# Kernel optimization log

Hardware: AMD Instinct MI355X
Metric: run time of the kernel (lower is better)

## Reference

```python
import jax, jax.numpy as jnp
import numpy as np

OBS_LEN = 8
PRED_LEN = 12
BATCH = 65536
EMB = 64
H = 64


def setup_inputs() -> dict:
    key = jax.random.key(0)
    ks = jax.random.split(key, 18)
    s = 1.0 / np.sqrt(H)  # torch default uniform bound scale, used as std here

    def p(k, shape):
        return (jax.random.normal(k, shape, dtype=jnp.float32) * s).astype(jnp.float32)

    return {
        "obs_traj": jax.random.normal(ks[0], (OBS_LEN, BATCH, 2), dtype=jnp.float32),
        "obs_traj_rel": jax.random.normal(ks[1], (OBS_LEN, BATCH, 2), dtype=jnp.float32),
        # encoder params
        "enc_emb_w": p(ks[2], (EMB, 2)),
        "enc_emb_b": p(ks[3], (EMB,)),
        "enc_w_ih": p(ks[4], (4 * H, EMB)),
        "enc_w_hh": p(ks[5], (4 * H, H)),
        "enc_b_ih": p(ks[6], (4 * H,)),
        "enc_b_hh": p(ks[7], (4 * H,)),
        # decoder params
        "dec_emb_w": p(ks[8], (EMB, 2)),
        "dec_emb_b": p(ks[9], (EMB,)),
        "dec_w_ih": p(ks[10], (4 * H, EMB)),
        "dec_w_hh": p(ks[11], (4 * H, H)),
        "dec_b_ih": p(ks[12], (4 * H,)),
        "dec_b_hh": p(ks[13], (4 * H,)),
        "h2p_w": p(ks[14], (2, H)),
        "h2p_b": p(ks[15], (2,)),
    }


def _lstm_cell(h, c, x, w_ih, w_hh, b_ih, b_hh):
    # torch nn.LSTM gate order: i, f, g, o
    gates = x @ w_ih.T + h @ w_hh.T + (b_ih + b_hh)
    i, f, g, o = jnp.split(gates, 4, axis=-1)
    c_new = jax.nn.sigmoid(f) * c + jax.nn.sigmoid(i) * jnp.tanh(g)
    h_new = jax.nn.sigmoid(o) * jnp.tanh(c_new)
    return h_new, c_new


def reference(obs_traj, obs_traj_rel,
              enc_emb_w, enc_emb_b, enc_w_ih, enc_w_hh, enc_b_ih, enc_b_hh,
              dec_emb_w, dec_emb_b, dec_w_ih, dec_w_hh, dec_b_ih, dec_b_hh,
              h2p_w, h2p_b):
    batch = obs_traj_rel.shape[1]

    # ---------- Encoder ----------
    enc_in = obs_traj_rel @ enc_emb_w.T + enc_emb_b  # [T, B, EMB]

    def enc_step(carry, x_t):
        h, c = carry
        h, c = _lstm_cell(h, c, x_t, enc_w_ih, enc_w_hh, enc_b_ih, enc_b_hh)
        return (h, c), None

    h0 = jnp.zeros((batch, H), dtype=obs_traj_rel.dtype)
    c0 = jnp.zeros((batch, H), dtype=obs_traj_rel.dtype)
    (h_enc, _), _ = jax.lax.scan(enc_step, (h0, c0), enc_in)

    # ---------- Decoder ----------
    dec_h = h_enc                                   # final encoder hidden seeds decoder
    dec_c = jnp.zeros((batch, H), dtype=obs_traj_rel.dtype)
    last_pos_rel = obs_traj_rel[-1]
    dec_in = last_pos_rel @ dec_emb_w.T + dec_emb_b  # [B, EMB]

    def dec_step(carry, _):
        h, c, x = carry
        h, c = _lstm_cell(h, c, x, dec_w_ih, dec_w_hh, dec_b_ih, dec_b_hh)
        rel_pos = h @ h2p_w.T + h2p_b               # [B, 2]
        x_next = rel_pos @ dec_emb_w.T + dec_emb_b  # [B, EMB]
        return (h, c, x_next), rel_pos

    (_, _, _), pred_traj_fake_rel = jax.lax.scan(
        dec_step, (dec_h, dec_c, dec_in), None, length=PRED_LEN)
    return pred_traj_fake_rel  # [PRED_LEN, B, 2]
```

## Files before the change

kernel.cpp:

```cpp
#include <hip/hip_runtime.h>

#define OBS_LEN 8
#define PRED_LEN 12
#define TILE_B 64
#define NTHREADS 256

typedef __attribute__((ext_vector_type(8))) short short8;
typedef __attribute__((ext_vector_type(4))) float floatx4;
typedef __attribute__((ext_vector_type(2))) float floatx2;
typedef __attribute__((ext_vector_type(2))) unsigned int u32x2;
typedef unsigned short u16;
typedef unsigned int u32;

#define L2E 1.442695040888963f

__device__ __forceinline__ u16 f2bf(float f) {
  __bf16 b = (__bf16)f;
  return __builtin_bit_cast(u16, b);
}

#if __has_builtin(__builtin_amdgcn_exp2f)
__device__ __forceinline__ float fexp2_(float x) { return __builtin_amdgcn_exp2f(x); }
#else
__device__ __forceinline__ float fexp2_(float x) { return exp2f(x); }
#endif
__device__ __forceinline__ floatx2 exp2v(floatx2 x) {
  floatx2 r;
  r.x = fexp2_(x.x);
  r.y = fexp2_(x.y);
  return r;
}
#if __has_builtin(__builtin_amdgcn_rcpf)
__device__ __forceinline__ floatx2 rcp2(floatx2 x) {
  floatx2 r;
  r.x = __builtin_amdgcn_rcpf(x.x);
  r.y = __builtin_amdgcn_rcpf(x.y);
  return r;
}
#else
__device__ __forceinline__ floatx2 rcp2(floatx2 x) {
  return floatx2{1.0f / x.x, 1.0f / x.y};
}
#endif

__device__ __forceinline__ floatx4 mfma_bf(short8 a, short8 b, floatx4 c) {
  return __builtin_amdgcn_mfma_f32_16x16x32_bf16(a, b, c, 0, 0, 0);
}

__device__ __forceinline__ void load_afrags(const float* __restrict__ W,
                                            short8 (&af)[4][2],
                                            int u0, int q, int l16) {
#pragma unroll
  for (int t = 0; t < 4; ++t)
#pragma unroll
    for (int kf = 0; kf < 2; ++kf) {
      const float* src = W + (t * 64 + u0 + l16) * 64 + kf * 32 + q * 8;
      const floatx4 w0 = *(const floatx4*)src;
      const floatx4 w1 = *(const floatx4*)(src + 4);
      short8 a;
#pragma unroll
      for (int j = 0; j < 4; ++j) {
        a[j] = (short)f2bf(w0[j]);
        a[j + 4] = (short)f2bf(w1[j]);
      }
      af[t][kf] = a;
    }
}

__device__ __forceinline__ void load_afrags_eff(const float* __restrict__ Whh,
                                                const float* __restrict__ aS0,
                                                const float* __restrict__ aS1,
                                                const float* __restrict__ hw0,
                                                const float* __restrict__ hw1,
                                                short8 (&af)[4][2],
                                                int u0, int q, int l16) {
#pragma unroll
  for (int t = 0; t < 4; ++t) {
    const int g = t * 64 + u0 + l16;
    const float a0 = aS0[g], a1 = aS1[g];
#pragma unroll
    for (int kf = 0; kf < 2; ++kf) {
      const int u = kf * 32 + q * 8;
      const float* src = Whh + g * 64 + u;
      const floatx4 w0 = *(const floatx4*)src;
      const floatx4 w1 = *(const floatx4*)(src + 4);
      const floatx4 p00 = *(const floatx4*)(hw0 + u);
      const floatx4 p01 = *(const floatx4*)(hw0 + u + 4);
      const floatx4 p10 = *(const floatx4*)(hw1 + u);
      const floatx4 p11 = *(const floatx4*)(hw1 + u + 4);
      short8 a;
#pragma unroll
      for (int j = 0; j < 4; ++j) {
        a[j] = (short)f2bf(w0[j] + a0 * p00[j] + a1 * p10[j]);
        a[j + 4] = (short)f2bf(w1[j] + a0 * p01[j] + a1 * p11[j]);
      }
      af[t][kf] = a;
    }
  }
}

__device__ __forceinline__ void fold_rank2(const float* __restrict__ wr,
                                           const float* __restrict__ emb_w,
                                           const float* __restrict__ emb_b,
                                           float& A0, float& A1, float& B0) {
  A0 = A1 = B0 = 0.f;
#pragma unroll
  for (int e4 = 0; e4 < 16; ++e4) {
    const floatx4 w = *(const floatx4*)(wr + e4 * 4);
    const floatx4 m0 = *(const floatx4*)(emb_w + e4 * 8);
    const floatx4 m1 = *(const floatx4*)(emb_w + e4 * 8 + 4);
    const floatx4 bb = *(const floatx4*)(emb_b + e4 * 4);
    A0 += w[0] * m0[0] + w[1] * m0[2] + w[2] * m1[0] + w[3] * m1[2];
    A1 += w[0] * m0[1] + w[1] * m0[3] + w[2] * m1[1] + w[3] * m1[3];
    B0 += w[0] * bb[0] + w[1] * bb[1] + w[2] * bb[2] + w[3] * bb[3];
  }
}

__device__ __forceinline__ void build_gfrag(const float* __restrict__ A0t,
                                            const float* __restrict__ A1t,
                                            short8 (&xf)[4],
                                            int u0, int q, int l16) {
#pragma unroll
  for (int t = 0; t < 4; ++t) {
    short8 a = short8{0, 0, 0, 0, 0, 0, 0, 0};
    if (q == 0) {
      const int g = t * 64 + u0 + l16;
      a[0] = (short)f2bf(A0t[g]);
      a[1] = (short)f2bf(A1t[g]);
    }
    xf[t] = a;
  }
}

__device__ __forceinline__ void nonlin_store(const floatx4 (&acc)[4],
                                             floatx2 (&c2)[2],
                                             u16* __restrict__ wrh,
                                             int s, int q, int wv) {
  const int sw = s & 7;
  u32 hpk[2];
#pragma unroll
  for (int p = 0; p < 2; ++p) {
    const floatx2 iv = {acc[0][2 * p], acc[0][2 * p + 1]};
    const floatx2 fv = {acc[1][2 * p], acc[1][2 * p + 1]};
    const floatx2 gv = {acc[2][2 * p], acc[2][2 * p + 1]};
    const floatx2 ov = {acc[3][2 * p], acc[3][2 * p + 1]};
    const floatx2 ei = exp2v(iv * -L2E);
    const floatx2 ef = exp2v(fv * -L2E);
    const floatx2 eg = exp2v(gv * (2.0f * L2E));
    const floatx2 eo = exp2v(ov * -L2E);
    const floatx2 A = ei + 1.0f;
    const floatx2 F = ef + 1.0f;
    const floatx2 Bg = eg + 1.0f;
    const floatx2 P = A * Bg;
    const floatx2 num = c2[p] * P + (eg - 1.0f) * F;
    const floatx2 cn = num * rcp2(F * P);
    c2[p] = cn;
    const floatx2 ec = exp2v(cn * (2.0f * L2E));
    const floatx2 h = (ec - 1.0f) * rcp2((eo + 1.0f) * (ec + 1.0f));
    hpk[p] = (u32)f2bf(h.x) | ((u32)f2bf(h.y) << 16);
  }
  *(u32x2*)(wrh + s * 64 + (((wv * 2 + (q >> 1)) ^ sw) * 8) + (q & 1) * 4) =
      u32x2{hpk[0], hpk[1]};
}

__device__ __forceinline__ void cell_step_fold(
    const u16* __restrict__ rdh, u16* __restrict__ wrh,
    const short8 (&afh)[4][2], const short8 (&xf)[4],
    const float* __restrict__ biasrow, const float* __restrict__ posrow,
    floatx2 (&c)[4][2], int q, int l16, int wv, int u0) {
#pragma unroll
  for (int n = 0; n < 4; ++n) {
    const int s = n * 16 + l16, sw = s & 7;
    const u16* hr = rdh + s * 64;
    const short8 hb0 = *(const short8*)(hr + ((q ^ sw) * 8));
    const short8 hb1 = *(const short8*)(hr + (((q + 4) ^ sw) * 8));
    const floatx2 pp = *(const floatx2*)(posrow + s * 2);
    short8 pf = short8{0, 0, 0, 0, 0, 0, 0, 0};
    if (q == 0) {
      pf[0] = (short)f2bf(pp.x);
      pf[1] = (short)f2bf(pp.y);
    }
    floatx4 acc[4];
#pragma unroll
    for (int t = 0; t < 4; ++t) {
      const floatx4 bias = *(const floatx4*)(biasrow + t * 64 + u0 + q * 4);
      acc[t] = mfma_bf(xf[t], pf, bias);
    }
#pragma unroll
    for (int t = 0; t < 4; ++t) acc[t] = mfma_bf(afh[t][0], hb0, acc[t]);
#pragma unroll
    for (int t = 0; t < 4; ++t) acc[t] = mfma_bf(afh[t][1], hb1, acc[t]);
    nonlin_store(acc, c[n], wrh, s, q, wv);
  }
}

__device__ __forceinline__ void dec_step_folded(
    const u16* __restrict__ rdh, u16* __restrict__ wrh,
    const short8 (&af)[4][2], const short8 (&xf)[4],
    const float* __restrict__ biasrow, float b2p0, float b2p1,
    float* __restrict__ relrow,
    floatx2 (&c)[4][2], int q, int l16, int wv, int u0) {
#pragma unroll
  for (int n = 0; n < 4; ++n) {
    const int s = n * 16 + l16, sw = s & 7;
    const u16* hr = rdh + s * 64;
    const short8 hb0 = *(const short8*)(hr + ((q ^ sw) * 8));
    const short8 hb1 = *(const short8*)(hr + (((q + 4) ^ sw) * 8));
    floatx4 acc[4];
#pragma unroll
    for (int t = 0; t < 4; ++t) {
      const floatx4 bias = *(const floatx4*)(biasrow + t * 64 + u0 + q * 4);
      acc[t] = mfma_bf(af[t][0], hb0, bias);
    }
#pragma unroll
    for (int t = 0; t < 4; ++t) acc[t] = mfma_bf(af[t][1], hb1, acc[t]);
    if (wv == n) {
      floatx4 ar = mfma_bf(xf[0], hb0, floatx4{0.f, 0.f, 0.f, 0.f});
      ar = mfma_bf(xf[1], hb1, ar);
      if (q == 0)
        *(floatx2*)(relrow + s * 2) = floatx2{ar[0] + b2p0, ar[1] + b2p1};
    }
    nonlin_store(acc, c[n], wrh, s, q, wv);
  }
}

__global__ void __launch_bounds__(NTHREADS, 4)
lstm_kernel(const float* __restrict__ obs_rel,
            const float* __restrict__ enc_emb_w, const float* __restrict__ enc_emb_b,
            const float* __restrict__ enc_w_ih, const float* __restrict__ enc_w_hh,
            const float* __restrict__ enc_b_ih, const float* __restrict__ enc_b_hh,
            const float* __restrict__ dec_emb_w, const float* __restrict__ dec_emb_b,
            const float* __restrict__ dec_w_ih, const float* __restrict__ dec_w_hh,
            const float* __restrict__ dec_b_ih, const float* __restrict__ dec_b_hh,
            const float* __restrict__ h2p_w, const float* __restrict__ h2p_b,
            float* __restrict__ out, int batch) {
  __shared__ __align__(16) u16 hS[2][TILE_B * 64];
  __shared__ __align__(16) float posS[OBS_LEN][TILE_B * 2];
  __shared__ __align__(16) float biasS[3][256];
  __shared__ __align__(16) float eA0[256], eA1[256];
  __shared__ __align__(16) float dA0[256], dA1[256];
  __shared__ __align__(16) float hw0S[64], hw1S[64];
  __shared__ __align__(16) float relS[PRED_LEN][TILE_B * 2];

  const int tid = threadIdx.x;
  const int wv = tid >> 6, lane = tid & 63;
  const int q = lane >> 4, l16 = lane & 15;
  const int u0 = wv << 4;
  const long S0 = (long)blockIdx.x * TILE_B;

  {
    const int t = tid >> 5, i = tid & 31;
    *(floatx4*)&posS[t][i * 4] =
        *(const floatx4*)(obs_rel + (long)t * batch * 2 + S0 * 2 + i * 4);
  }
  if (tid < 64) {
    hw0S[tid] = h2p_w[tid];
    hw1S[tid] = h2p_w[64 + tid];
  }
  {
    float A0, A1, B0;
    fold_rank2(enc_w_ih + tid * 64, enc_emb_w, enc_emb_b, A0, A1, B0);
    eA0[tid] = A0;
    eA1[tid] = A1;
    biasS[0][tid] = enc_b_ih[tid] + enc_b_hh[tid] + B0;
    fold_rank2(dec_w_ih + tid * 64, dec_emb_w, dec_emb_b, A0, A1, B0);
    dA0[tid] = A0;
    dA1[tid] = A1;
    const float db = dec_b_ih[tid] + dec_b_hh[tid] + B0;
    biasS[1][tid] = db;
    biasS[2][tid] = db + A0 * h2p_b[0] + A1 * h2p_b[1];
  }
  for (int i = tid; i < TILE_B * 64 / 2; i += NTHREADS) ((u32*)&hS[0][0])[i] = 0;

  short8 afh[4][2], xf[4];
  floatx2 c[4][2];
  load_afrags(enc_w_hh, afh, u0, q, l16);
#pragma unroll
  for (int n = 0; n < 4; ++n) c[n][0] = c[n][1] = floatx2{0.f, 0.f};
  const float b2p0 = h2p_b[0], b2p1 = h2p_b[1];
  __syncthreads();
  build_gfrag(eA0, eA1, xf, u0, q, l16);

  int pb = 0;
#pragma unroll 1
  for (int t = 0; t < OBS_LEN; ++t) {
    cell_step_fold(hS[pb], hS[pb ^ 1], afh, xf, &biasS[0][0], &posS[t][0], c,
                   q, l16, wv, u0);
    __syncthreads();
    pb ^= 1;
  }

  load_afrags(dec_w_hh, afh, u0, q, l16);
  build_gfrag(dA0, dA1, xf, u0, q, l16);
#pragma unroll
  for (int n = 0; n < 4; ++n) c[n][0] = c[n][1] = floatx2{0.f, 0.f};
  cell_step_fold(hS[pb], hS[pb ^ 1], afh, xf, &biasS[1][0], &posS[7][0], c,
                 q, l16, wv, u0);
  load_afrags_eff(dec_w_hh, dA0, dA1, hw0S, hw1S, afh, u0, q, l16);
#pragma unroll
  for (int kf = 0; kf < 2; ++kf) {
    const int kb = kf * 32 + q * 8;
    short8 a;
#pragma unroll
    for (int j = 0; j < 4; ++j) {
      const float r0 = (l16 == 0) ? hw0S[kb + j] : (l16 == 1) ? hw1S[kb + j] : 0.f;
      const float r1 =
          (l16 == 0) ? hw0S[kb + 4 + j] : (l16 == 1) ? hw1S[kb + 4 + j] : 0.f;
      a[j] = (short)f2bf(r0);
      a[j + 4] = (short)f2bf(r1);
    }
    xf[kf] = a;
  }
  __syncthreads();
  pb ^= 1;

#pragma unroll 1
  for (int j = 1; j < PRED_LEN; ++j) {
    dec_step_folded(hS[pb], hS[pb ^ 1], afh, xf, &biasS[2][0], b2p0, b2p1,
                    &relS[j - 1][0], c, q, l16, wv, u0);
    __syncthreads();
    pb ^= 1;
  }

  {
    const int s = wv * 16 + l16, sw = s & 7;
    const u16* hr = hS[pb] + s * 64;
    const short8 ha = *(const short8*)(hr + ((q ^ sw) * 8));
    const short8 hc = *(const short8*)(hr + (((q + 4) ^ sw) * 8));
    floatx4 ar = mfma_bf(xf[0], ha, floatx4{0.f, 0.f, 0.f, 0.f});
    ar = mfma_bf(xf[1], hc, ar);
    if (q == 0)
      *(floatx2*)(&relS[PRED_LEN - 1][s * 2]) =
          floatx2{ar[0] + b2p0, ar[1] + b2p1};
  }
  __syncthreads();

#pragma unroll
  for (int r = 0; r < 6; ++r) {
    const int f = tid + r * 256;
    const int j = f >> 7, e = f & 127;
    out[(long)j * batch * 2 + S0 * 2 + e] = ((const float*)relS)[f];
  }
}

extern "C" void kernel_launch(void* const* d_in, const int* in_sizes, int n_in,
                              void* d_out, int out_size, void* d_ws, size_t ws_size,
                              hipStream_t stream) {
  const float* obs_rel = (const float*)d_in[1];
  const int batch = in_sizes[1] / (OBS_LEN * 2);

  const int blocks = batch / TILE_B;
  hipLaunchKernelGGL(lstm_kernel, dim3(blocks), dim3(NTHREADS), 0, stream,
                     obs_rel,
                     (const float*)d_in[2], (const float*)d_in[3],
                     (const float*)d_in[4], (const float*)d_in[5],
                     (const float*)d_in[6], (const float*)d_in[7],
                     (const float*)d_in[8], (const float*)d_in[9],
                     (const float*)d_in[10], (const float*)d_in[11],
                     (const float*)d_in[12], (const float*)d_in[13],
                     (const float*)d_in[14], (const float*)d_in[15],
                     (float*)d_out, batch);
}
```

Baseline: 200.0 us.

## Give each wave its own batch rows and stage weight fragments in LDS

Each wave now owns 16 batch rows and computes all 256 gate units for them, so the hidden state lives in a per-wave LDS region. This removes the per-timestep __syncthreads barriers. Weight fragments are pre-swizzled into shared memory and read per MFMA rather than held in registers, and the launch bound drops from 4 to 3 blocks per SM. Predictions are written straight to global memory instead of being staged in LDS. The trade-off is more LDS traffic per step and lower occupancy, in exchange for fewer barriers and less register pressure.

Measured after the change: 197.7 us. Within noise of the previous version (-1.2%).

```diff
diff --git a/kernel.cpp b/kernel.cpp
--- a/kernel.cpp
+++ b/kernel.cpp
@@ -8,6 +8,7 @@
 typedef __attribute__((ext_vector_type(8))) short short8;
 typedef __attribute__((ext_vector_type(4))) float floatx4;
 typedef __attribute__((ext_vector_type(2))) float floatx2;
+typedef __attribute__((ext_vector_type(4))) unsigned int u32x4;
 typedef __attribute__((ext_vector_type(2))) unsigned int u32x2;
 typedef unsigned short u16;
 typedef unsigned int u32;
@@ -47,56 +48,8 @@
   return __builtin_amdgcn_mfma_f32_16x16x32_bf16(a, b, c, 0, 0, 0);
 }
 
-__device__ __forceinline__ void load_afrags(const float* __restrict__ W,
-                                            short8 (&af)[4][2],
-                                            int u0, int q, int l16) {
-#pragma unroll
-  for (int t = 0; t < 4; ++t)
-#pragma unroll
-    for (int kf = 0; kf < 2; ++kf) {
-      const float* src = W + (t * 64 + u0 + l16) * 64 + kf * 32 + q * 8;
-      const floatx4 w0 = *(const floatx4*)src;
-      const floatx4 w1 = *(const floatx4*)(src + 4);
-      short8 a;
-#pragma unroll
-      for (int j = 0; j < 4; ++j) {
-        a[j] = (short)f2bf(w0[j]);
-        a[j + 4] = (short)f2bf(w1[j]);
-      }
-      af[t][kf] = a;
-    }
-}
-
-__device__ __forceinline__ void load_afrags_eff(const float* __restrict__ Whh,
-                                                const float* __restrict__ aS0,
-                                                const float* __restrict__ aS1,
-                                                const float* __restrict__ hw0,
-                                                const float* __restrict__ hw1,
-                                                short8 (&af)[4][2],
-                                                int u0, int q, int l16) {
-#pragma unroll
-  for (int t = 0; t < 4; ++t) {
-    const int g = t * 64 + u0 + l16;
-    const float a0 = aS0[g], a1 = aS1[g];
-#pragma unroll
-    for (int kf = 0; kf < 2; ++kf) {
-      const int u = kf * 32 + q * 8;
-      const float* src = Whh + g * 64 + u;
-      const floatx4 w0 = *(const floatx4*)src;
-      const floatx4 w1 = *(const floatx4*)(src + 4);
-      const floatx4 p00 = *(const floatx4*)(hw0 + u);
-      const floatx4 p01 = *(const floatx4*)(hw0 + u + 4);
-      const floatx4 p10 = *(const floatx4*)(hw1 + u);
-      const floatx4 p11 = *(const floatx4*)(hw1 + u + 4);
-      short8 a;
-#pragma unroll
-      for (int j = 0; j < 4; ++j) {
-        a[j] = (short)f2bf(w0[j] + a0 * p00[j] + a1 * p10[j]);
-        a[j + 4] = (short)f2bf(w1[j] + a0 * p01[j] + a1 * p11[j]);
-      }
-      af[t][kf] = a;
-    }
-  }
+__device__ __forceinline__ short8 frag_lo(u32 a) {
+  return __builtin_bit_cast(short8, u32x4{a, 0u, 0u, 0u});
 }
 
 __device__ __forceinline__ void fold_rank2(const float* __restrict__ wr,
@@ -116,27 +69,63 @@
   }
 }
 
-__device__ __forceinline__ void build_gfrag(const float* __restrict__ A0t,
-                                            const float* __restrict__ A1t,
-                                            short8 (&xf)[4],
-                                            int u0, int q, int l16) {
-#pragma unroll
-  for (int t = 0; t < 4; ++t) {
-    short8 a = short8{0, 0, 0, 0, 0, 0, 0, 0};
-    if (q == 0) {
-      const int g = t * 64 + u0 + l16;
-      a[0] = (short)f2bf(A0t[g]);
-      a[1] = (short)f2bf(A1t[g]);
+__device__ __forceinline__ void stage_w(const float* __restrict__ W,
+                                        u16* __restrict__ wS, int tid) {
+#pragma unroll
+  for (int i = 0; i < 8; ++i) {
+    const int slot = tid + i * 256;
+    const int lane = slot & 63, kf = (slot >> 6) & 1, tile = slot >> 7;
+    const int g = lane >> 4, l16 = lane & 15;
+    const int gate = (tile >> 2) * 64 + (tile & 3) * 16 + l16;
+    const float* src = W + gate * 64 + kf * 32 + g * 8;
+    const floatx4 w0 = *(const floatx4*)src;
+    const floatx4 w1 = *(const floatx4*)(src + 4);
+    short8 a;
+#pragma unroll
+    for (int j = 0; j < 4; ++j) {
+      a[j] = (short)f2bf(w0[j]);
+      a[j + 4] = (short)f2bf(w1[j]);
     }
-    xf[t] = a;
-  }
-}
-
-__device__ __forceinline__ void nonlin_store(const floatx4 (&acc)[4],
-                                             floatx2 (&c2)[2],
-                                             u16* __restrict__ wrh,
-                                             int s, int q, int wv) {
-  const int sw = s & 7;
+    *(short8*)(wS + slot * 8) = a;
+  }
+}
+
+__device__ __forceinline__ void stage_weff(const float* __restrict__ Whh,
+                                           const float* __restrict__ dA0S,
+                                           const float* __restrict__ dA1S,
+                                           const float* __restrict__ hw0,
+                                           const float* __restrict__ hw1,
+                                           u16* __restrict__ wS, int tid) {
+#pragma unroll
+  for (int i = 0; i < 8; ++i) {
+    const int slot = tid + i * 256;
+    const int lane = slot & 63, kf = (slot >> 6) & 1, tile = slot >> 7;
+    const int g = lane >> 4, l16 = lane & 15;
+    const int gate = (tile >> 2) * 64 + (tile & 3) * 16 + l16;
+    const int k0 = kf * 32 + g * 8;
+    const float a0 = dA0S[gate], a1 = dA1S[gate];
+    const float* src = Whh + gate * 64 + k0;
+    const floatx4 w0 = *(const floatx4*)src;
+    const floatx4 w1 = *(const floatx4*)(src + 4);
+    const floatx4 p00 = *(const floatx4*)(hw0 + k0);
+    const floatx4 p01 = *(const floatx4*)(hw0 + k0 + 4);
+    const floatx4 p10 = *(const floatx4*)(hw1 + k0);
+    const floatx4 p11 = *(const floatx4*)(hw1 + k0 + 4);
+    short8 a;
+#pragma unroll
+    for (int j = 0; j < 4; ++j) {
+      a[j] = (short)f2bf(w0[j] + a0 * p00[j] + a1 * p10[j]);
+      a[j + 4] = (short)f2bf(w1[j] + a0 * p01[j] + a1 * p11[j]);
+    }
+    *(short8*)(wS + slot * 8) = a;
+  }
+}
+
+__device__ __forceinline__ void nonlin_store_ut(const floatx4 (&acc)[4],
+                                                floatx4& cc,
+                                                u16* __restrict__ wrh,
+                                                int l16, int g, int ut) {
+  const int sw = l16 & 7;
   u32 hpk[2];
 #pragma unroll
   for (int p = 0; p < 2; ++p) {
@@ -152,79 +141,45 @@
     const floatx2 F = ef + 1.0f;
     const floatx2 Bg = eg + 1.0f;
     const floatx2 P = A * Bg;
-    const floatx2 num = c2[p] * P + (eg - 1.0f) * F;
+    const floatx2 cold = {cc[2 * p], cc[2 * p + 1]};
+    const floatx2 num = cold * P + (eg - 1.0f) * F;
     const floatx2 cn = num * rcp2(F * P);
-    c2[p] = cn;
+    cc[2 * p] = cn.x;
+    cc[2 * p + 1] = cn.y;
     const floatx2 ec = exp2v(cn * (2.0f * L2E));
     const floatx2 h = (ec - 1.0f) * rcp2((eo + 1.0f) * (ec + 1.0f));
     hpk[p] = (u32)f2bf(h.x) | ((u32)f2bf(h.y) << 16);
   }
-  *(u32x2*)(wrh + s * 64 + (((wv * 2 + (q >> 1)) ^ sw) * 8) + (q & 1) * 4) =
+  *(u32x2*)(wrh + l16 * 64 + (((ut * 2 + (g >> 1)) ^ sw) * 8) + (g & 1) * 4) =
       u32x2{hpk[0], hpk[1]};
 }
 
-__device__ __forceinline__ void cell_step_fold(
-    const u16* __restrict__ rdh, u16* __restrict__ wrh,
-    const short8 (&afh)[4][2], const short8 (&xf)[4],
-    const float* __restrict__ biasrow, const float* __restrict__ posrow,
-    floatx2 (&c)[4][2], int q, int l16, int wv, int u0) {
-#pragma unroll
-  for (int n = 0; n < 4; ++n) {
-    const int s = n * 16 + l16, sw = s & 7;
-    const u16* hr = rdh + s * 64;
-    const short8 hb0 = *(const short8*)(hr + ((q ^ sw) * 8));
-    const short8 hb1 = *(const short8*)(hr + (((q + 4) ^ sw) * 8));
-    const floatx2 pp = *(const floatx2*)(posrow + s * 2);
-    short8 pf = short8{0, 0, 0, 0, 0, 0, 0, 0};
-    if (q == 0) {
-      pf[0] = (short)f2bf(pp.x);
-      pf[1] = (short)f2bf(pp.y);
+template <int PH>
+__device__ __forceinline__ void ut_group(int ut, floatx4& cc,
+                                         short8 hb0, short8 hb1, short8 pfv,
+                                         const u16* __restrict__ wp,
+                                         const u32* __restrict__ pafp,
+                                         const float* __restrict__ biasp,
+                                         u16* __restrict__ wrh,
+                                         int g, int l16) {
+  floatx4 acc[4];
+#pragma unroll
+  for (int tg = 0; tg < 4; ++tg) {
+    const int tile = tg * 4 + ut;
+    const floatx4 biasv = *(const floatx4*)(biasp + tg * 64 + ut * 16 + g * 4);
+    if (PH == 0) {
+      const u32 pa = (g == 0) ? pafp[tile * 16 + l16] : 0u;
+      acc[tg] = mfma_bf(frag_lo(pa), pfv, biasv);
+    } else {
+      acc[tg] = biasv;
     }
-    floatx4 acc[4];
-#pragma unroll
-    for (int t = 0; t < 4; ++t) {
-      const floatx4 bias = *(const floatx4*)(biasrow + t * 64 + u0 + q * 4);
-      acc[t] = mfma_bf(xf[t], pf, bias);
-    }
-#pragma unroll
-    for (int t = 0; t < 4; ++t) acc[t] = mfma_bf(afh[t][0], hb0, acc[t]);
-#pragma unroll
-    for (int t = 0; t < 4; ++t) acc[t] = mfma_bf(afh[t][1], hb1, acc[t]);
-    nonlin_store(acc, c[n], wrh, s, q, wv);
-  }
-}
-
-__device__ __forceinline__ void dec_step_folded(
-    const u16* __restrict__ rdh, u16* __restrict__ wrh,
-    const short8 (&af)[4][2], const short8 (&xf)[4],
-    const float* __restrict__ biasrow, float b2p0, float b2p1,
-    float* __restrict__ relrow,
-    floatx2 (&c)[4][2], int q, int l16, int wv, int u0) {
-#pragma unroll
-  for (int n = 0; n < 4; ++n) {
-    const int s = n * 16 + l16, sw = s & 7;
-    const u16* hr = rdh + s * 64;
-    const short8 hb0 = *(const short8*)(hr + ((q ^ sw) * 8));
-    const short8 hb1 = *(const short8*)(hr + (((q + 4) ^ sw) * 8));
-    floatx4 acc[4];
-#pragma unroll
-    for (int t = 0; t < 4; ++t) {
-      const floatx4 bias = *(const floatx4*)(biasrow + t * 64 + u0 + q * 4);
-      acc[t] = mfma_bf(af[t][0], hb0, bias);
-    }
-#pragma unroll
-    for (int t = 0; t < 4; ++t) acc[t] = mfma_bf(af[t][1], hb1, acc[t]);
-    if (wv == n) {
-      floatx4 ar = mfma_bf(xf[0], hb0, floatx4{0.f, 0.f, 0.f, 0.f});
-      ar = mfma_bf(xf[1], hb1, ar);
-      if (q == 0)
-        *(floatx2*)(relrow + s * 2) = floatx2{ar[0] + b2p0, ar[1] + b2p1};
-    }
-    nonlin_store(acc, c[n], wrh, s, q, wv);
-  }
-}
-
-__global__ void __launch_bounds__(NTHREADS, 4)
+    acc[tg] = mfma_bf(*(const short8*)(wp + (tile * 2 + 1) * 512), hb1, acc[tg]);
+    acc[tg] = mfma_bf(*(const short8*)(wp + (tile * 2 + 0) * 512), hb0, acc[tg]);
+  }
+  nonlin_store_ut(acc, cc, wrh, l16, g, ut);
+}
+
+__global__ void __launch_bounds__(NTHREADS, 3)
 lstm_kernel(const float* __restrict__ obs_rel,
             const float* __restrict__ enc_emb_w, const float* __restrict__ enc_emb_b,
             const float* __restrict__ enc_w_ih, const float* __restrict__ enc_w_hh,
@@ -234,112 +189,134 @@
             const float* __restrict__ dec_b_ih, const float* __restrict__ dec_b_hh,
             const float* __restrict__ h2p_w, const float* __restrict__ h2p_b,
             float* __restrict__ out, int batch) {
-  __shared__ __align__(16) u16 hS[2][TILE_B * 64];
-  __shared__ __align__(16) float posS[OBS_LEN][TILE_B * 2];
+  __shared__ __align__(16) u16 wS[16384];
+  __shared__ __align__(16) u16 hP[4 * 1024];
   __shared__ __align__(16) float biasS[3][256];
-  __shared__ __align__(16) float eA0[256], eA1[256];
-  __shared__ __align__(16) float dA0[256], dA1[256];
+  __shared__ __align__(16) u32 pafS[2][256];
+  __shared__ __align__(16) u32 posP[OBS_LEN * 64];
   __shared__ __align__(16) float hw0S[64], hw1S[64];
-  __shared__ __align__(16) float relS[PRED_LEN][TILE_B * 2];
+  __shared__ __align__(16) float dA0S[256], dA1S[256];
 
   const int tid = threadIdx.x;
   const int wv = tid >> 6, lane = tid & 63;
-  const int q = lane >> 4, l16 = lane & 15;
-  const int u0 = wv << 4;
+  const int g = lane >> 4, l16 = lane & 15;
   const long S0 = (long)blockIdx.x * TILE_B;
 
-  {
-    const int t = tid >> 5, i = tid & 31;
-    *(floatx4*)&posS[t][i * 4] =
-        *(const floatx4*)(obs_rel + (long)t * batch * 2 + S0 * 2 + i * 4);
+  for (int i = tid; i < OBS_LEN * 64; i += NTHREADS) {
+    const int t = i >> 6, s = i & 63;
+    const floatx2 pp = *(const floatx2*)(obs_rel + (long)t * batch * 2 + (S0 + s) * 2);
+    posP[i] = (u32)f2bf(pp.x) | ((u32)f2bf(pp.y) << 16);
   }
   if (tid < 64) {
     hw0S[tid] = h2p_w[tid];
     hw1S[tid] = h2p_w[64 + tid];
   }
+  const float hb2p0 = h2p_b[0], hb2p1 = h2p_b[1];
   {
+    const int t = tid >> 6, u6 = tid & 63;
+    const int pidx = (t * 4 + (u6 >> 4)) * 16 + (u6 & 15);
     float A0, A1, B0;
     fold_rank2(enc_w_ih + tid * 64, enc_emb_w, enc_emb_b, A0, A1, B0);
-    eA0[tid] = A0;
-    eA1[tid] = A1;
+    pafS[0][pidx] = (u32)f2bf(A0) | ((u32)f2bf(A1) << 16);
     biasS[0][tid] = enc_b_ih[tid] + enc_b_hh[tid] + B0;
     fold_rank2(dec_w_ih + tid * 64, dec_emb_w, dec_emb_b, A0, A1, B0);
-    dA0[tid] = A0;
-    dA1[tid] = A1;
+    pafS[1][pidx] = (u32)f2bf(A0) | ((u32)f2bf(A1) << 16);
+    dA0S[tid] = A0;
+    dA1S[tid] = A1;
     const float db = dec_b_ih[tid] + dec_b_hh[tid] + B0;
     biasS[1][tid] = db;
-    biasS[2][tid] = db + A0 * h2p_b[0] + A1 * h2p_b[1];
-  }
-  for (int i = tid; i < TILE_B * 64 / 2; i += NTHREADS) ((u32*)&hS[0][0])[i] = 0;
-
-  short8 afh[4][2], xf[4];
-  floatx2 c[4][2];
-  load_afrags(enc_w_hh, afh, u0, q, l16);
-#pragma unroll
-  for (int n = 0; n < 4; ++n) c[n][0] = c[n][1] = floatx2{0.f, 0.f};
-  const float b2p0 = h2p_b[0], b2p1 = h2p_b[1];
-  __syncthreads();
-  build_gfrag(eA0, eA1, xf, u0, q, l16);
-
-  int pb = 0;
+    biasS[2][tid] = db + A0 * hb2p0 + A1 * hb2p1;
+  }
+  stage_w(enc_w_hh, wS, tid);
+  for (int i = tid; i < 2048; i += NTHREADS) ((u32*)hP)[i] = 0;
+  __syncthreads();
+
+  u16* hw = hP + wv * 1024;
+  const u16* wp = wS + lane * 8;
+  const int sw8 = l16 & 7;
+  floatx4 c0{0.f, 0.f, 0.f, 0.f}, c1{0.f, 0.f, 0.f, 0.f};
+  floatx4 c2v{0.f, 0.f, 0.f, 0.f}, c3{0.f, 0.f, 0.f, 0.f};
+
 #pragma unroll 1
   for (int t = 0; t < OBS_LEN; ++t) {
-    cell_step_fold(hS[pb], hS[pb ^ 1], afh, xf, &biasS[0][0], &posS[t][0], c,
-                   q, l16, wv, u0);
-    __syncthreads();
-    pb ^= 1;
-  }
-
-  load_afrags(dec_w_hh, afh, u0, q, l16);
-  build_gfrag(dA0, dA1, xf, u0, q, l16);
-#pragma unroll
-  for (int n = 0; n < 4; ++n) c[n][0] = c[n][1] = floatx2{0.f, 0.f};
-  cell_step_fold(hS[pb], hS[pb ^ 1], afh, xf, &biasS[1][0], &posS[7][0], c,
-                 q, l16, wv, u0);
-  load_afrags_eff(dec_w_hh, dA0, dA1, hw0S, hw1S, afh, u0, q, l16);
+    const u16* hr = hw + l16 * 64;
+    const short8 hb0 = *(const short8*)(hr + ((g ^ sw8) * 8));
+    const short8 hb1 = *(const short8*)(hr + (((4 + g) ^ sw8) * 8));
+    const u32 pp = (g == 0) ? posP[t * 64 + wv * 16 + l16] : 0u;
+    const short8 pfv = frag_lo(pp);
+    ut_group<0>(0, c0, hb0, hb1, pfv, wp, &pafS[0][0], &biasS[0][0], hw, g, l16);
+    __builtin_amdgcn_sched_barrier(0);
+    ut_group<0>(1, c1, hb0, hb1, pfv, wp, &pafS[0][0], &biasS[0][0], hw, g, l16);
+    __builtin_amdgcn_sched_barrier(0);
+    ut_group<0>(2, c2v, hb0, hb1, pfv, wp, &pafS[0][0], &biasS[0][0], hw, g, l16);
+    __builtin_amdgcn_sched_barrier(0);
+    ut_group<0>(3, c3, hb0, hb1, pfv, wp, &pafS[0][0], &biasS[0][0], hw, g, l16);
+  }
+
+  __syncthreads();
+  stage_w(dec_w_hh, wS, tid);
+  __syncthreads();
+  c0 = c1 = c2v = c3 = floatx4{0.f, 0.f, 0.f, 0.f};
+  {
+    const u16* hr = hw + l16 * 64;
+    const short8 hb0 = *(const short8*)(hr + ((g ^ sw8) * 8));
+    const short8 hb1 = *(const short8*)(hr + (((4 + g) ^ sw8) * 8));
+    const u32 pp = (g == 0) ? posP[7 * 64 + wv * 16 + l16] : 0u;
+    const short8 pfv = frag_lo(pp);
+    ut_group<0>(0, c0, hb0, hb1, pfv, wp, &pafS[1][0], &biasS[1][0], hw, g, l16);
+    __builtin_amdgcn_sched_barrier(0);
+    ut_group<0>(1, c1, hb0, hb1, pfv, wp, &pafS[1][0], &biasS[1][0], hw, g, l16);
+    __builtin_amdgcn_sched_barrier(0);
+    ut_group<0>(2, c2v, hb0, hb1, pfv, wp, &pafS[1][0], &biasS[1][0], hw, g, l16);
+    __builtin_amdgcn_sched_barrier(0);
+    ut_group<0>(3, c3, hb0, hb1, pfv, wp, &pafS[1][0], &biasS[1][0], hw, g, l16);
+  }
+  __syncthreads();
+  stage_weff(dec_w_hh, dA0S, dA1S, hw0S, hw1S, wS, tid);
+  __syncthreads();
+
+  short8 xf0, xf1;
 #pragma unroll
   for (int kf = 0; kf < 2; ++kf) {
-    const int kb = kf * 32 + q * 8;
+    const int kb = kf * 32 + g * 8;
     short8 a;
 #pragma unroll
-    for (int j = 0; j < 4; ++j) {
-      const float r0 = (l16 == 0) ? hw0S[kb + j] : (l16 == 1) ? hw1S[kb + j] : 0.f;
-      const float r1 =
-          (l16 == 0) ? hw0S[kb + 4 + j] : (l16 == 1) ? hw1S[kb + 4 + j] : 0.f;
-      a[j] = (short)f2bf(r0);
-      a[j + 4] = (short)f2bf(r1);
+    for (int j = 0; j < 8; ++j) {
+      const float r = (l16 == 0) ? hw0S[kb + j] : (l16 == 1) ? hw1S[kb + j] : 0.f;
+      a[j] = (short)f2bf(r);
     }
-    xf[kf] = a;
-  }
-  __syncthreads();
-  pb ^= 1;
-
+    if (kf == 0) xf0 = a; else xf1 = a;
+  }
+
+  const floatx4 zero4{0.f, 0.f, 0.f, 0.f};
 #pragma unroll 1
   for (int j = 1; j < PRED_LEN; ++j) {
-    dec_step_folded(hS[pb], hS[pb ^ 1], afh, xf, &biasS[2][0], b2p0, b2p1,
-                    &relS[j - 1][0], c, q, l16, wv, u0);
-    __syncthreads();
-    pb ^= 1;
+    const u16* hr = hw + l16 * 64;
+    const short8 hb0 = *(const short8*)(hr + ((g ^ sw8) * 8));
+    const short8 hb1 = *(const short8*)(hr + (((4 + g) ^ sw8) * 8));
+    floatx4 ar = mfma_bf(xf0, hb0, zero4);
+    ar = mfma_bf(xf1, hb1, ar);
+    if (g == 0)
+      *(floatx2*)(out + (long)(j - 1) * batch * 2 + (S0 + wv * 16 + l16) * 2) =
+          floatx2{ar[0] + hb2p0, ar[1] + hb2p1};
+    ut_group<1>(0, c0, hb0, hb1, xf0, wp, &pafS[1][0], &biasS[2][0], hw, g, l16);
+    __builtin_amdgcn_sched_barrier(0);
+    ut_group<1>(1, c1, hb0, hb1, xf0, wp, &pafS[1][0], &biasS[2][0], hw, g, l16);
+    __builtin_amdgcn_sched_barrier(0);
+    ut_group<1>(2, c2v, hb0, hb1, xf0, wp, &pafS[1][0], &biasS[2][0], hw, g, l16);
+    __builtin_amdgcn_sched_barrier(0);
+    ut_group<1>(3, c3, hb0, hb1, xf0, wp, &pafS[1][0], &biasS[2][0], hw, g, l16);
   }
 
   {
-    const int s = wv * 16 + l16, sw = s & 7;
-    const u16* hr = hS[pb] + s * 64;
-    const short8 ha = *(const short8*)(hr + ((q ^ sw) * 8));
-    const short8 hc = *(const short8*)(hr + (((q + 4) ^ sw) * 8));
-    floatx4 ar = mfma_bf(xf[0], ha, floatx4{0.f, 0.f, 0.f, 0.f});
-    ar = mfma_bf(xf[1], hc, ar);
-    if (q == 0)
-      *(floatx2*)(&relS[PRED_LEN - 1][s * 2]) =
-          floatx2{ar[0] + b2p0, ar[1] + b2p1};
-  }
-  __syncthreads();
-
-#pragma unroll
-  for (int r = 0; r < 6; ++r) {
-    const int f = tid + r * 256;
-    const int j = f >> 7, e = f & 127;
-    out[(long)j * batch * 2 + S0 * 2 + e] = ((const float*)relS)[f];
+    const u16* hr = hw + l16 * 64;
+    const short8 hb0 = *(const short8*)(hr + ((g ^ sw8) * 8));
+    const short8 hb1 = *(const short8*)(hr + (((4 + g) ^ sw8) * 8));
+    floatx4 ar = mfma_bf(xf0, hb0, zero4);
+    ar = mfma_bf(xf1, hb1, ar);
+    if (g == 0)
+      *(floatx2*)(out + (long)(PRED_LEN - 1) * batch * 2 + (S0 + wv * 16 + l16) * 2) =
+          floatx2{ar[0] + hb2p0, ar[1] + hb2p1};
   }
 }
 
```
